# Kernel tuning notes

Measured on AMD Instinct MI355X. Metric: run time of the kernel, lower is better.

The kernel has to match this reference:

```python
import jax, jax.numpy as jnp
import numpy as np

D_MODEL = 1024
N_HEADS = 16
D_K = D_MODEL // N_HEADS
MIN_F = 3
MAX_F = 10


def setup_inputs() -> dict:
    key = jax.random.key(0)
    ks = jax.random.split(key, 9)
    B, L = 4, 8192
    x = jax.random.normal(ks[0], (B, L, D_MODEL), jnp.float32)
    def w(k):
        return jax.random.normal(k, (D_MODEL, D_MODEL), jnp.float32) * 0.02
    def b(k):
        return jax.random.normal(k, (D_MODEL,), jnp.float32) * 0.02
    return {
        'x': x,
        'wq': w(ks[1]), 'bq': b(ks[2]),
        'wk': w(ks[3]), 'bk': b(ks[4]),
        'wv': w(ks[5]), 'bv': b(ks[6]),
        'wo': w(ks[7]), 'bo': b(ks[8]),
    }


def _sparsity_score(Q):
    # Q: (B, H, L, d_k)
    l2 = jnp.linalg.norm(Q, axis=-1)
    logp = jax.nn.log_softmax(Q, axis=-1)
    prob = jnp.exp(logp)
    entropy = -jnp.sum(prob * jnp.log(prob + 1e-9), axis=-1)
    var = jnp.var(Q, axis=-1, ddof=1)  # torch.var is unbiased by default
    return 0.5 * l2 + 0.3 * entropy + 0.2 * var


def reference(x, wq, bq, wk, bk, wv, bv, wo, bo):
    B, L, D = x.shape
    H, dk = N_HEADS, D_K
    # torch Linear: y = x @ W.T + b
    Q = (x @ wq.T + bq).reshape(B, L, H, dk).transpose(0, 2, 1, 3)  # (B,H,L,dk)
    K = (x @ wk.T + bk).reshape(B, L, H, dk).transpose(0, 2, 1, 3)
    V = (x @ wv.T + bv).reshape(B, L, H, dk).transpose(0, 2, 1, 3)

    q_scores = _sparsity_score(Q)  # (B,H,L)
    q_std = jnp.std(q_scores, axis=2, keepdims=True, ddof=1)
    q_mean = jnp.mean(q_scores, axis=2, keepdims=True)
    factor = jnp.clip(
        jnp.round(q_std / (q_mean + 1e-6) * MAX_F).astype(jnp.int32),
        MIN_F, MAX_F)  # (B,H,1)
    u = factor[:, 0, 0]  # per-batch k, taken from head 0 (matches torch code)

    # Fixed-size top-k of MAX_F; rows beyond u are masked to zero.
    _, top_idx = jax.lax.top_k(q_scores, MAX_F)  # (B,H,MAX_F)
    mask = (jnp.arange(MAX_F)[None, None, :] < u[:, None, None])  # (B,1->H,MAX_F)

    Q_sparse = jnp.take_along_axis(Q, top_idx[..., None], axis=2)  # (B,H,MAX_F,dk)
    scores = jnp.einsum('bhud,bhld->bhul', Q_sparse, K) / np.sqrt(dk).astype(np.float32)
    attn = jax.nn.softmax(scores, axis=-1)
    out = jnp.einsum('bhul,bhld->bhud', attn, V)  # (B,H,MAX_F,dk)
    out = out * mask[..., None].astype(out.dtype)

    # Scatter back into zeros; top-k indices are distinct per (b,h), so writing
    # masked zeros at the extra indices leaves those rows zero as in torch.
    bi = jnp.arange(B)[:, None, None]
    hi = jnp.arange(H)[None, :, None]
    full = jnp.zeros((B, H, L, dk), out.dtype).at[bi, hi, top_idx].set(out)

    merged = full.transpose(0, 2, 1, 3).reshape(B, L, D)
    return merged @ wo.T + bo
```

## Files before the change

kernel.cpp:

```cpp
#include <hip/hip_runtime.h>
#include <cmath>


typedef short     s16x8 __attribute__((ext_vector_type(8)));
typedef unsigned short u16x8 __attribute__((ext_vector_type(8)));
typedef unsigned short u16x4 __attribute__((ext_vector_type(4)));
typedef float     f32x4 __attribute__((ext_vector_type(4)));

__device__ __forceinline__ unsigned short f2bf(float f) {
    unsigned u = __float_as_uint(f);
    u += 0x7fffu + ((u >> 16) & 1u);
    return (unsigned short)(u >> 16);
}
__device__ __forceinline__ float bf2f(unsigned short s) {
    return __uint_as_float(((unsigned)s) << 16);
}

__device__ __forceinline__ void async16(const void* g, void* l) {
    __builtin_amdgcn_global_load_lds(
        (const __attribute__((address_space(1))) void*)g,
        (__attribute__((address_space(3))) void*)l, 16, 0, 0);
}

__global__ void k_conv(const float* __restrict__ x, const float* __restrict__ wq,
                       const float* __restrict__ wk, const float* __restrict__ wv,
                       unsigned short* __restrict__ xb, unsigned short* __restrict__ wb) {
    size_t i = (size_t)blockIdx.x * 256 + threadIdx.x;
    if (i < 8388608) {
        float4 v = ((const float4*)x)[i];
        ushort4 o; o.x = f2bf(v.x); o.y = f2bf(v.y); o.z = f2bf(v.z); o.w = f2bf(v.w);
        ((ushort4*)xb)[i] = o;
    } else {
        size_t j = i - 8388608;
        size_t wsel = j >> 18, rem = j & 262143;
        const float* src = wsel == 0 ? wq : (wsel == 1 ? wk : wv);
        float4 v = ((const float4*)src)[rem];
        ushort4 o; o.x = f2bf(v.x); o.y = f2bf(v.y); o.z = f2bf(v.z); o.w = f2bf(v.w);
        ((ushort4*)wb)[j] = o;
    }
}

__device__ __forceinline__ void rdA(s16x8 (&dst)[2][2], const char* A_, int r0,
                                    int qk0, int qk1) {
    dst[0][0] = *(const s16x8*)(A_ + r0 * 2048 + qk0);
    dst[0][1] = *(const s16x8*)(A_ + r0 * 2048 + qk1);
    dst[1][0] = *(const s16x8*)(A_ + (r0 + 1) * 2048 + qk0);
    dst[1][1] = *(const s16x8*)(A_ + (r0 + 1) * 2048 + qk1);
}
__device__ __forceinline__ void mfma8(f32x4 (&acc)[8][4], int i0, int i1,
                                      const s16x8 (&aa)[2][2], const s16x8 (&bfr)[4][2]) {
    __builtin_amdgcn_s_setprio(1);
#pragma unroll
    for (int kk = 0; kk < 2; ++kk)
#pragma unroll
        for (int n = 0; n < 4; ++n) {
            acc[i0][n] = __builtin_amdgcn_mfma_f32_16x16x32_bf16(aa[0][kk], bfr[n][kk], acc[i0][n], 0, 0, 0);
            acc[i1][n] = __builtin_amdgcn_mfma_f32_16x16x32_bf16(aa[1][kk], bfr[n][kk], acc[i1][n], 0, 0, 0);
        }
    __builtin_amdgcn_s_setprio(0);
}

__global__ __launch_bounds__(512, 2) void k_gemm_qkv(
    const unsigned short* __restrict__ xb, const unsigned short* __restrict__ wb,
    const float* __restrict__ bq, const float* __restrict__ bk, const float* __restrict__ bv,
    unsigned short* __restrict__ Kb, unsigned short* __restrict__ Vb,
    float* __restrict__ scores)
{
    extern __shared__ char ldsb[];
    int bid = blockIdx.x;
    int mt = bid / 12, ntile = bid % 12;
    int wsel = ntile >> 2, ntq = ntile & 3;
    int tid = threadIdx.x, wid = tid >> 6, lane = tid & 63;
    int wm = wid >> 2, wn = wid & 3;
    int ml = lane & 15, quad = lane >> 4;

    const char* xg = (const char*)(xb + (size_t)mt * 256 * 1024);
    const char* wg = (const char*)(wb + (size_t)ntile * 256 * 1024);

    int rg0  = wid * 2;
    int rsub = lane >> 3;
    int cswz = ((lane & 7) ^ rsub) << 4;

#define STAGE(gbase_, roff_) do {                                          \
        const char* _g = (gbase_) + (size_t)(rg0 * 8 + rsub) * 2048 + cswz; \
        char* _l = ldsb + (roff_) + rg0 * 1024;                             \
        async16(_g, _l);                                                    \
        async16(_g + 8 * 2048, _l + 1024);                                  \
    } while (0)

    int q0  = (quad * 16) ^ ((ml & 7) << 4);
    int qk0 = q0, qk1 = q0 ^ 64;
    int aconst = wm * 16384 + ml * 128;
    int bconst = 32768 + (wn >> 1) * 16384 + (wn & 1) * 8192 + ml * 128;

    f32x4 acc[8][4] = {};

    STAGE(wg,                32768);
    STAGE(wg + 262144,       32768 + 16384);
    STAGE(xg,                0);
    STAGE(xg + 262144,       16384);
    STAGE(wg + 128,          65536 + 32768);
    STAGE(wg + 262144 + 128, 65536 + 32768 + 16384);
    asm volatile("s_waitcnt vmcnt(4)" ::: "memory");
    __builtin_amdgcn_s_barrier();
    asm volatile("" ::: "memory");

    for (int t = 0; t < 16; ++t) {
        int buf  = (t & 1) << 16;
        int nbuf = buf ^ 65536;
        const char* A_ = ldsb + buf + aconst;
        const char* B_ = ldsb + buf + bconst;
        s16x8 bfr[4][2];
#pragma unroll
        for (int n = 0; n < 4; ++n) {
            bfr[n][0] = *(const s16x8*)(B_ + n * 2048 + qk0);
            bfr[n][1] = *(const s16x8*)(B_ + n * 2048 + qk1);
        }
        s16x8 af[2][2], ag[2][2];
        rdA(af, A_, 0, qk0, qk1);
        if (t < 15) STAGE(xg + (size_t)(t + 1) * 128, nbuf);
        rdA(ag, A_, 2, qk0, qk1);
        mfma8(acc, 0, 1, af, bfr);
        if (t < 15) STAGE(xg + 262144 + (size_t)(t + 1) * 128, nbuf + 16384);
        rdA(af, A_, 4, qk0, qk1);
        mfma8(acc, 2, 3, ag, bfr);
        asm volatile("" ::: "memory");
        __builtin_amdgcn_s_barrier();
        asm volatile("" ::: "memory");
        if (t < 14) STAGE(wg + (size_t)(t + 2) * 128, buf + 32768);
        rdA(ag, A_, 6, qk0, qk1);
        mfma8(acc, 4, 5, af, bfr);
        if (t < 14) STAGE(wg + 262144 + (size_t)(t + 2) * 128, buf + 32768 + 16384);
        mfma8(acc, 6, 7, ag, bfr);
        if (t <= 13)      asm volatile("s_waitcnt vmcnt(4)" ::: "memory");
        else if (t == 14) asm volatile("s_waitcnt vmcnt(0)" ::: "memory");
        asm volatile("" ::: "memory");
        __builtin_amdgcn_s_barrier();
        asm volatile("" ::: "memory");
    }
#undef STAGE

    float bvv[4];
    const float* bias = wsel == 0 ? bq : (wsel == 1 ? bk : bv);
    int colbase = ntq * 256 + wn * 64;
#pragma unroll
    for (int n = 0; n < 4; ++n) bvv[n] = bias[colbase + n * 16 + ml];

    if (wsel == 0) {
        int hh = ntq * 4 + wn;
#pragma unroll
        for (int m = 0; m < 8; ++m) {
#pragma unroll
            for (int r = 0; r < 4; ++r) {
                float q0v = acc[m][0][r] + bvv[0];
                float q1v = acc[m][1][r] + bvv[1];
                float q2v = acc[m][2][r] + bvv[2];
                float q3v = acc[m][3][r] + bvv[3];
                float mx = fmaxf(fmaxf(q0v, q1v), fmaxf(q2v, q3v));
                float sm = q0v + q1v + q2v + q3v;
                float ss = q0v * q0v + q1v * q1v + q2v * q2v + q3v * q3v;
#pragma unroll
                for (int off = 1; off < 16; off <<= 1) {
                    mx = fmaxf(mx, __shfl_xor(mx, off));
                    sm += __shfl_xor(sm, off);
                    ss += __shfl_xor(ss, off);
                }
                float e0 = expf(q0v - mx), e1 = expf(q1v - mx);
                float e2 = expf(q2v - mx), e3 = expf(q3v - mx);
                float S = e0 + e1 + e2 + e3;
#pragma unroll
                for (int off = 1; off < 16; off <<= 1) S += __shfl_xor(S, off);
                float is = 1.f / S;
                float p0 = e0 * is, p1 = e1 * is, p2 = e2 * is, p3 = e3 * is;
                float ent = -p0 * logf(p0 + 1e-9f) - p1 * logf(p1 + 1e-9f)
                            - p2 * logf(p2 + 1e-9f) - p3 * logf(p3 + 1e-9f);
                float mean = sm * (1.f / 64.f);
                float d0 = q0v - mean, d1 = q1v - mean, d2 = q2v - mean, d3 = q3v - mean;
                float var = d0 * d0 + d1 * d1 + d2 * d2 + d3 * d3;
#pragma unroll
                for (int off = 1; off < 16; off <<= 1) {
                    ent += __shfl_xor(ent, off);
                    var += __shfl_xor(var, off);
                }
                if (ml == 0) {
                    float sc = 0.5f * sqrtf(ss) + 0.3f * ent + 0.2f * (var * (1.f / 63.f));
                    int row = mt * 256 + wm * 128 + m * 16 + quad * 4 + r;
                    scores[(size_t)(((row >> 13) << 4) + hh) * 8192 + (row & 8191)] = sc;
                }
            }
        }
    } else {
        unsigned short* outp = wsel == 1 ? Kb : Vb;
#pragma unroll
        for (int m = 0; m < 8; ++m) {
            int grow0 = mt * 256 + wm * 128 + m * 16 + quad * 4;
#pragma unroll
            for (int n = 0; n < 4; ++n) {
                int gcol = colbase + n * 16 + ml;
#pragma unroll
                for (int r = 0; r < 4; ++r)
                    outp[(size_t)(grow0 + r) * 1024 + gcol] = f2bf(acc[m][n][r] + bvv[n]);
            }
        }
    }
}

__global__ __launch_bounds__(1024) void k_cand(const float* __restrict__ scores,
                                               int* __restrict__ cand, int* __restrict__ u)
{
    int pair = blockIdx.x; int t = threadIdx.x;
    __shared__ float  s_lds[8192];
    __shared__ double dred[1024];
    __shared__ float  wvv[16];
    __shared__ int    wii[16];
    const float* sp = scores + (size_t)pair * 8192;
    for (int i = t; i < 8192; i += 1024) s_lds[i] = sp[i];
    __syncthreads();

    if ((pair & 15) == 0) {
        double a0 = 0;
#pragma unroll
        for (int k = 0; k < 8; ++k) a0 += (double)s_lds[t + k * 1024];
        dred[t] = a0; __syncthreads();
        for (int st = 512; st > 0; st >>= 1) { if (t < st) dred[t] += dred[t + st]; __syncthreads(); }
        double mean = dred[0] / 8192.0;
        __syncthreads();
        double a1 = 0;
#pragma unroll
        for (int k = 0; k < 8; ++k) { double d = (double)s_lds[t + k * 1024] - mean; a1 += d * d; }
        dred[t] = a1; __syncthreads();
        for (int st = 512; st > 0; st >>= 1) { if (t < st) dred[t] += dred[t + st]; __syncthreads(); }
        if (t == 0) {
            double sd = sqrt(dred[0] / 8191.0);
            double ratio = sd / (mean + 1e-6) * 10.0;
            int f = (int)rint(ratio);
            f = f < 3 ? 3 : (f > 10 ? 10 : f);
            u[pair >> 4] = f;
        }
        __syncthreads();
    }

    for (int it = 0; it < 16; ++it) {
        float bv = -1e30f; int bi = 0x7fffffff;
#pragma unroll
        for (int k = 0; k < 8; ++k) {
            int i = t + k * 1024;
            float v = s_lds[i];
            if (v > bv || (v == bv && i < bi)) { bv = v; bi = i; }
        }
#pragma unroll
        for (int off = 32; off > 0; off >>= 1) {
            float ov = __shfl_down(bv, off);
            int   oi = __shfl_down(bi, off);
            if (ov > bv || (ov == bv && oi < bi)) { bv = ov; bi = oi; }
        }
        if ((t & 63) == 0) { wvv[t >> 6] = bv; wii[t >> 6] = bi; }
        __syncthreads();
        if (t == 0) {
            float fv = wvv[0]; int fi = wii[0];
            for (int k = 1; k < 16; ++k)
                if (wvv[k] > fv || (wvv[k] == fv && wii[k] < fi)) { fv = wvv[k]; fi = wii[k]; }
            cand[pair * 16 + it] = fi;
            s_lds[fi] = -1e30f;
        }
        __syncthreads();
    }
}

__global__ __launch_bounds__(256) void k_rescore(
    const int* __restrict__ cand, const float* __restrict__ x,
    const float* __restrict__ wq, const float* __restrict__ bq,
    double* __restrict__ cscore, float* __restrict__ cq)
{
    int bid = blockIdx.x;
    int pair = bid >> 4;
    int b = pair >> 4, h = pair & 15;
    int t = threadIdx.x;
    __shared__ float  xrow[1024];
    __shared__ double dred[256];
    __shared__ double qrow[64];

    int l = cand[bid];
    const float* xr = x + ((size_t)b * 8192 + l) * 1024;
    for (int i = t; i < 1024; i += 256) xrow[i] = xr[i];
    __syncthreads();

    int d = t >> 2, ks = t & 3;
    const float* wr = wq + (size_t)(h * 64 + d) * 1024 + ks * 256;
    const float* xs = xrow + ks * 256;
    double p = 0;
    for (int k = 0; k < 256; k += 4) {
        float4 w4 = *(const float4*)(wr + k);
        float4 x4 = *(const float4*)(xs + k);
        p += (double)w4.x * x4.x + (double)w4.y * x4.y +
             (double)w4.z * x4.z + (double)w4.w * x4.w;
    }
    dred[t] = p; __syncthreads();
    if ((t & 3) == 0)
        qrow[t >> 2] = dred[t] + dred[t + 1] + dred[t + 2] + dred[t + 3] + (double)bq[h * 64 + (t >> 2)];
    __syncthreads();

    if (t < 64) {
        double q = qrow[t];
        cq[(size_t)bid * 64 + t] = (float)q;
        double m = q;
#pragma unroll
        for (int off = 32; off > 0; off >>= 1) m = fmax(m, __shfl_down(m, off));
        m = __shfl(m, 0);
        double e = exp(q - m);
        double sum = q, sumsq = q * q, S = e;
#pragma unroll
        for (int off = 32; off > 0; off >>= 1) {
            sum += __shfl_down(sum, off);
            sumsq += __shfl_down(sumsq, off);
            S += __shfl_down(S, off);
        }
        sum = __shfl(sum, 0); sumsq = __shfl(sumsq, 0); S = __shfl(S, 0);
        double pp = e / S;
        double entc = -pp * log(pp + 1e-9);
        double mean = sum / 64.0;
        double dv = q - mean;
        double varc = dv * dv;
#pragma unroll
        for (int off = 32; off > 0; off >>= 1) {
            entc += __shfl_down(entc, off);
            varc += __shfl_down(varc, off);
        }
        if (t == 0)
            cscore[bid] = 0.5 * sqrt(sumsq) + 0.3 * entc + 0.2 * (varc / 63.0);
    }
}

__global__ void k_select(const int* __restrict__ cand, const double* __restrict__ cscore,
                         const float* __restrict__ cq,
                         int* __restrict__ sel, float* __restrict__ selq)
{
    int pair = blockIdx.x; int t = threadIdx.x;
    __shared__ int order[10];
    if (t == 0) {
        bool used[16] = {};
        for (int r = 0; r < 10; ++r) {
            int best = -1;
            for (int c = 0; c < 16; ++c) {
                if (used[c]) continue;
                int ic = pair * 16 + c;
                if (best < 0 || cscore[ic] > cscore[pair * 16 + best] ||
                    (cscore[ic] == cscore[pair * 16 + best] && cand[ic] < cand[pair * 16 + best]))
                    best = c;
            }
            used[best] = true; order[r] = best;
            sel[pair * 10 + r] = cand[pair * 16 + best];
        }
    }
    __syncthreads();
    for (int r = 0; r < 10; ++r)
        selq[((size_t)pair * 10 + r) * 64 + t] = cq[((size_t)pair * 16 + order[r]) * 64 + t];
}

__global__ __launch_bounds__(256) void k_attn_part(
    const unsigned short* __restrict__ Kb, const unsigned short* __restrict__ Vb,
    const float* __restrict__ selq, const int* __restrict__ u,
    float* __restrict__ part)
{
    int bid = blockIdx.x;
    int pair = bid >> 5, chunk = bid & 31;
    int b = pair >> 4, h = pair & 15;
    int uu = u[b];
    int t = threadIdx.x, wave = t >> 6, lane = t & 63;

    __shared__ float q_sh[10][64];
    __shared__ float w_sh[10][256];
    __shared__ unsigned short V_sh[256][68];
    __shared__ float mc_sh[10][2], Sc_sh[10][2];

    size_t kvbase = ((size_t)b * 8192 + (size_t)chunk * 256) * 1024 + h * 64;

    for (int i = t; i < uu * 64; i += 256)
        q_sh[i >> 6][i & 63] = selq[(size_t)pair * 640 + i] * 0.125f;

    const u16x8* kr = (const u16x8*)(Kb + kvbase + (size_t)t * 1024);
    const u16x8* vr = (const u16x8*)(Vb + kvbase + (size_t)t * 1024);
    u16x8 vreg[8];
#pragma unroll
    for (int k8 = 0; k8 < 8; ++k8) vreg[k8] = vr[k8];
#pragma unroll
    for (int k8 = 0; k8 < 8; ++k8) {
        *(u16x4*)&V_sh[t][k8 * 8]     = { vreg[k8][0], vreg[k8][1], vreg[k8][2], vreg[k8][3] };
        *(u16x4*)&V_sh[t][k8 * 8 + 4] = { vreg[k8][4], vreg[k8][5], vreg[k8][6], vreg[k8][7] };
    }
    float krow[64];
#pragma unroll
    for (int k8 = 0; k8 < 8; ++k8) {
        u16x8 kv = kr[k8];
#pragma unroll
        for (int e = 0; e < 8; ++e) krow[k8 * 8 + e] = bf2f(kv[e]);
    }
    __syncthreads();

    for (int rr = 0; rr < uu; ++rr) {
        const float4* qp = (const float4*)q_sh[rr];
        float acc = 0.f;
#pragma unroll
        for (int i4 = 0; i4 < 16; ++i4) {
            float4 q4 = qp[i4];
            acc += q4.x * krow[i4 * 4] + q4.y * krow[i4 * 4 + 1] +
                   q4.z * krow[i4 * 4 + 2] + q4.w * krow[i4 * 4 + 3];
        }
        w_sh[rr][t] = acc;
    }
    __syncthreads();

    for (int rr = wave; rr < uu; rr += 4) {
        float4 wv = *(const float4*)&w_sh[rr][lane * 4];
        float m4 = fmaxf(fmaxf(wv.x, wv.y), fmaxf(wv.z, wv.w));
#pragma unroll
        for (int off = 16; off > 0; off >>= 1) m4 = fmaxf(m4, __shfl_xor(m4, off));
        float e0 = expf(wv.x - m4), e1 = expf(wv.y - m4);
        float e2 = expf(wv.z - m4), e3 = expf(wv.w - m4);
        float s = e0 + e1 + e2 + e3;
#pragma unroll
        for (int off = 16; off > 0; off >>= 1) s += __shfl_xor(s, off);
        float4 ev = { e0, e1, e2, e3 };
        *(float4*)&w_sh[rr][lane * 4] = ev;
        if ((lane & 31) == 0) { int jh = lane >> 5; mc_sh[rr][jh] = m4; Sc_sh[rr][jh] = s; }
    }
    __syncthreads();

    int jh = t >> 7, tt = t & 127, dp = tt & 31;
    for (int rr = tt >> 5; rr < uu; rr += 4) {
        float o0 = 0.f, o1 = 0.f;
        int j0 = jh * 128;
        for (int j = j0; j < j0 + 128; j += 4) {
            float4 w4 = *(const float4*)&w_sh[rr][j];
#pragma unroll
            for (int jj = 0; jj < 4; ++jj) {
                unsigned v = *(const unsigned*)&V_sh[j + jj][dp * 2];
                float w1 = jj == 0 ? w4.x : (jj == 1 ? w4.y : (jj == 2 ? w4.z : w4.w));
                o0 += w1 * __uint_as_float(v << 16);
                o1 += w1 * __uint_as_float(v & 0xffff0000u);
            }
        }
        float* pp = part + (((size_t)pair * 10 + rr) * 64 + chunk * 2 + jh) * 66;
        float2 o2 = { o0, o1 };
        *(float2*)&pp[2 + dp * 2] = o2;
        if (dp == 0) { pp[0] = mc_sh[rr][jh]; pp[1] = Sc_sh[rr][jh]; }
    }
}

__global__ void k_bias(const float* __restrict__ bo, float* __restrict__ out) {
    size_t i = (size_t)blockIdx.x * 256 + threadIdx.x;
    int col4 = (int)(i & 255);
    ((float4*)out)[i] = ((const float4*)bo)[col4];
}

__global__ __launch_bounds__(256) void k_mergescatter(
    const float* __restrict__ part, const int* __restrict__ sel,
    const int* __restrict__ u, const float* __restrict__ wo,
    float* __restrict__ out)
{
    int idx = blockIdx.x; int pair = idx / 10; int r = idx % 10;
    int b = pair >> 4, h = pair & 15;
    if (r >= u[b]) return;
    int t = threadIdx.x;
    __shared__ float a_sh[64];
    if (t < 64) {
        const float* base = part + ((size_t)pair * 10 + r) * 64 * 66;
        float m = -1e30f;
        for (int c = 0; c < 64; ++c) m = fmaxf(m, base[c * 66]);
        float S = 0, o = 0;
        for (int c = 0; c < 64; ++c) {
            float f = expf(base[c * 66] - m);
            S += f * base[c * 66 + 1];
            o += f * base[c * 66 + 2 + t];
        }
        a_sh[t] = o / S;
    }
    __syncthreads();
    int l = sel[pair * 10 + r];
    float* orow = out + ((size_t)b * 8192 + l) * 1024;
    for (int j = t; j < 1024; j += 256) {
        const float* wr = wo + (size_t)j * 1024 + h * 64;
        float acc = 0;
#pragma unroll
        for (int d = 0; d < 64; d += 4) {
            float4 w4 = *(const float4*)(wr + d);
            acc += a_sh[d] * w4.x + a_sh[d + 1] * w4.y + a_sh[d + 2] * w4.z + a_sh[d + 3] * w4.w;
        }
        atomicAdd(orow + j, acc);
    }
}

static constexpr size_t OFF_XB    = 0;
static constexpr size_t OFF_WB    = OFF_XB + 67108864;
static constexpr size_t OFF_KB    = OFF_WB + 6291456;
static constexpr size_t OFF_VB    = OFF_KB + 67108864;
static constexpr size_t OFF_SC    = OFF_VB + 67108864;
static constexpr size_t OFF_U     = OFF_SC + 2097152;
static constexpr size_t OFF_SEL   = OFF_U + 256;
static constexpr size_t OFF_SELQ  = OFF_SEL + 4096;
static constexpr size_t OFF_PART  = OFF_SELQ + 163840;
static constexpr size_t OFF_CAND  = OFF_PART + 10813440;
static constexpr size_t OFF_CSC   = OFF_CAND + 4096;
static constexpr size_t OFF_CQ    = OFF_CSC + 8192;
static constexpr size_t WS_NEED   = OFF_CQ + 262144;

extern "C" void kernel_launch(void* const* d_in, const int* in_sizes, int n_in,
                              void* d_out, int out_size, void* d_ws, size_t ws_size,
                              hipStream_t stream)
{
    const float* x  = (const float*)d_in[0];
    const float* wq = (const float*)d_in[1];
    const float* bq = (const float*)d_in[2];
    const float* wk = (const float*)d_in[3];
    const float* bk = (const float*)d_in[4];
    const float* wv = (const float*)d_in[5];
    const float* bv = (const float*)d_in[6];
    const float* wo = (const float*)d_in[7];
    const float* bo = (const float*)d_in[8];
    float* out = (float*)d_out;

    if (ws_size < WS_NEED) return;

    char* ws = (char*)d_ws;
    unsigned short* xb = (unsigned short*)(ws + OFF_XB);
    unsigned short* wb = (unsigned short*)(ws + OFF_WB);
    unsigned short* Kb = (unsigned short*)(ws + OFF_KB);
    unsigned short* Vb = (unsigned short*)(ws + OFF_VB);
    float*  scores = (float*)(ws + OFF_SC);
    int*    u      = (int*)(ws + OFF_U);
    int*    sel    = (int*)(ws + OFF_SEL);
    float*  selq   = (float*)(ws + OFF_SELQ);
    float*  part   = (float*)(ws + OFF_PART);
    int*    cand   = (int*)(ws + OFF_CAND);
    double* cscore = (double*)(ws + OFF_CSC);
    float*  cq     = (float*)(ws + OFF_CQ);

    k_conv        <<<35840, 256,  0,      stream>>>(x, wq, wk, wv, xb, wb);
    k_gemm_qkv    <<<1536,  512,  131072, stream>>>(xb, wb, bq, bk, bv, Kb, Vb, scores);
    k_cand        <<<64,    1024, 0,      stream>>>(scores, cand, u);
    k_rescore     <<<1024,  256,  0,      stream>>>(cand, x, wq, bq, cscore, cq);
    k_select      <<<64,    64,   0,      stream>>>(cand, cscore, cq, sel, selq);
    k_attn_part   <<<2048,  256,  0,      stream>>>(Kb, Vb, selq, u, part);
    k_bias        <<<32768, 256,  0,      stream>>>(bo, out);
    k_mergescatter<<<640,   256,  0,      stream>>>(part, sel, u, wo, out);
}
```

Baseline: 710.3 us.

## Triple-buffer the A tile in the QKV GEMM to prefetch two K-steps ahead

The QKV projection GEMM now keeps three rotating LDS buffers for the x (A) tile and loads it two iterations ahead, while the weight (B) tile stays double-buffered in a separate region. Shared memory per block grows from 128 KiB to 160 KiB, and the wait count is raised so more global loads stay in flight. It also drops the redundant barrier after the final iteration. The aim is to hide global-to-LDS latency better, at the risk of hitting the LDS capacity limit or lowering occupancy.

Measured after the change: 697.6 us. Within noise of the previous version (-1.8%).

```diff
diff --git a/kernel.cpp b/kernel.cpp
--- a/kernel.cpp
+++ b/kernel.cpp
@@ -91,25 +91,28 @@
     int q0  = (quad * 16) ^ ((ml & 7) << 4);
     int qk0 = q0, qk1 = q0 ^ 64;
     int aconst = wm * 16384 + ml * 128;
-    int bconst = 32768 + (wn >> 1) * 16384 + (wn & 1) * 8192 + ml * 128;
+    int bconst = (wn >> 1) * 16384 + (wn & 1) * 8192 + ml * 128;
 
     f32x4 acc[8][4] = {};
 
-    STAGE(wg,                32768);
-    STAGE(wg + 262144,       32768 + 16384);
     STAGE(xg,                0);
     STAGE(xg + 262144,       16384);
-    STAGE(wg + 128,          65536 + 32768);
-    STAGE(wg + 262144 + 128, 65536 + 32768 + 16384);
-    asm volatile("s_waitcnt vmcnt(4)" ::: "memory");
+    STAGE(wg,                98304);
+    STAGE(wg + 262144,       98304 + 16384);
+    STAGE(xg + 128,          32768);
+    STAGE(xg + 262144 + 128, 32768 + 16384);
+    STAGE(wg + 128,          131072);
+    STAGE(wg + 262144 + 128, 131072 + 16384);
+    asm volatile("s_waitcnt vmcnt(8)" ::: "memory");
     __builtin_amdgcn_s_barrier();
     asm volatile("" ::: "memory");
 
+    int abase = 0;
+    int sbase = 65536;
     for (int t = 0; t < 16; ++t) {
-        int buf  = (t & 1) << 16;
-        int nbuf = buf ^ 65536;
-        const char* A_ = ldsb + buf + aconst;
-        const char* B_ = ldsb + buf + bconst;
+        int bbase = 98304 + ((t & 1) << 15);
+        const char* A_ = ldsb + abase + aconst;
+        const char* B_ = ldsb + bbase + bconst;
         s16x8 bfr[4][2];
 #pragma unroll
         for (int n = 0; n < 4; ++n) {
@@ -118,25 +121,29 @@
         }
         s16x8 af[2][2], ag[2][2];
         rdA(af, A_, 0, qk0, qk1);
-        if (t < 15) STAGE(xg + (size_t)(t + 1) * 128, nbuf);
+        if (t < 14) STAGE(xg + (size_t)(t + 2) * 128, sbase);
         rdA(ag, A_, 2, qk0, qk1);
         mfma8(acc, 0, 1, af, bfr);
-        if (t < 15) STAGE(xg + 262144 + (size_t)(t + 1) * 128, nbuf + 16384);
+        if (t < 14) STAGE(xg + 262144 + (size_t)(t + 2) * 128, sbase + 16384);
         rdA(af, A_, 4, qk0, qk1);
         mfma8(acc, 2, 3, ag, bfr);
         asm volatile("" ::: "memory");
         __builtin_amdgcn_s_barrier();
         asm volatile("" ::: "memory");
-        if (t < 14) STAGE(wg + (size_t)(t + 2) * 128, buf + 32768);
+        if (t < 14) STAGE(wg + (size_t)(t + 2) * 128, bbase);
         rdA(ag, A_, 6, qk0, qk1);
         mfma8(acc, 4, 5, af, bfr);
-        if (t < 14) STAGE(wg + 262144 + (size_t)(t + 2) * 128, buf + 32768 + 16384);
+        if (t < 14) STAGE(wg + 262144 + (size_t)(t + 2) * 128, bbase + 16384);
         mfma8(acc, 6, 7, ag, bfr);
-        if (t <= 13)      asm volatile("s_waitcnt vmcnt(4)" ::: "memory");
-        else if (t == 14) asm volatile("s_waitcnt vmcnt(0)" ::: "memory");
-        asm volatile("" ::: "memory");
-        __builtin_amdgcn_s_barrier();
-        asm volatile("" ::: "memory");
+        if (t < 15) {
+            if (t <= 13)      asm volatile("s_waitcnt vmcnt(8)" ::: "memory");
+            else              asm volatile("s_waitcnt vmcnt(0)" ::: "memory");
+            asm volatile("" ::: "memory");
+            __builtin_amdgcn_s_barrier();
+            asm volatile("" ::: "memory");
+        }
+        abase = abase == 65536 ? 0 : abase + 32768;
+        sbase = sbase == 65536 ? 0 : sbase + 32768;
     }
 #undef STAGE
 
@@ -536,7 +543,7 @@
     float*  cq     = (float*)(ws + OFF_CQ);
 
     k_conv        <<<35840, 256,  0,      stream>>>(x, wq, wk, wv, xb, wb);
-    k_gemm_qkv    <<<1536,  512,  131072, stream>>>(xb, wb, bq, bk, bv, Kb, Vb, scores);
+    k_gemm_qkv    <<<1536,  512,  163840, stream>>>(xb, wb, bq, bk, bv, Kb, Vb, scores);
     k_cand        <<<64,    1024, 0,      stream>>>(scores, cand, u);
     k_rescore     <<<1024,  256,  0,      stream>>>(cand, x, wq, bq, cscore, cq);
     k_select      <<<64,    64,   0,      stream>>>(cand, cscore, cq, sel, selq);
```
